# Performance work log

Hardware: AMD Instinct MI355X
Metric: run time of the kernel (lower is better)

Reference implementation:

```python
import jax, jax.numpy as jnp
import numpy as np

# kernel / loss hyperparameters (from base_params)
FIT_SIGMA = 1.0
FIT_L = 1.0
MMD_SIGMA = 1.0
MMD_L = 2.0
REG_LAMBDA = 0.01

N, D = 8192, 16


def setup_inputs() -> dict:
    key = jax.random.key(0)
    k1, k2, k3 = jax.random.split(key, 3)
    X = jax.random.normal(k1, (N, D), dtype=jnp.float32)
    Y = jax.random.normal(k2, (N, D), dtype=jnp.float32)
    Lam = jax.random.normal(k3, (N, D), dtype=jnp.float32)  # nn.init.normal_ on zeros(N,d)
    return {"X": X, "Y": Y, "Lam": Lam}


def _rbf_gram(X, sigma, l):
    # k(xi, xj) = sigma^2 * exp(-||xi - xj||^2 / (2 l^2)), vectorized over all pairs
    sq = jnp.sum(X * X, axis=1)                      # [N]
    d2 = sq[:, None] + sq[None, :] - 2.0 * (X @ X.T)  # [N, N] squared distances
    d2 = jnp.maximum(d2, 0.0)
    return (sigma ** 2) * jnp.exp(-d2 / (2.0 * l ** 2))


def reference(X, Y, Lam):
    fit_kXX = _rbf_gram(X, FIT_SIGMA, FIT_L)   # [N, N]
    mmd_kXX = _rbf_gram(X, MMD_SIGMA, MMD_L)   # [N, N]
    diff = fit_kXX @ Lam - Y                   # [N, d]
    # trace(diff^T K diff) = sum(diff * (K @ diff))
    loss_fit = jnp.sum(diff * (mmd_kXX @ diff))
    loss_reg = REG_LAMBDA * jnp.sum(Lam * (fit_kXX @ Lam))
    return loss_fit + loss_reg
```

## Files before the change

### kernel.cpp

```cpp
#include <hip/hip_runtime.h>

#define NPTS 8192
#define DIM  16

constexpr int BLK = 256;
constexpr int NIB = NPTS / BLK;

#define REG_LAMBDA 0.01f
#define C1 1.2011224087864498f
#define C2 0.6005612043932249f

typedef _Float16 h4 __attribute__((ext_vector_type(4)));
typedef float    f4 __attribute__((ext_vector_type(4)));

#define MFMA16(a, b, c) __builtin_amdgcn_mfma_f32_16x16x16f16((a), (b), (c), 0, 0, 0)

#if __has_builtin(__builtin_amdgcn_exp2f)
#define EXP2(x) __builtin_amdgcn_exp2f(x)
#else
#define EXP2(x) exp2f(x)
#endif

__device__ __forceinline__ float dot4(float4 a, float4 b) {
  return fmaf(a.x, b.x, fmaf(a.y, b.y, fmaf(a.z, b.z, a.w * b.w)));
}
__device__ __forceinline__ void add4(float4& a, float4 b) {
  a.x += b.x; a.y += b.y; a.z += b.z; a.w += b.w;
}

__device__ __forceinline__ float block_sum(float v, float* wbuf) {
#pragma unroll
  for (int o = 32; o > 0; o >>= 1) v += __shfl_down(v, o, 64);
  const int lane = threadIdx.x & 63;
  const int wid  = threadIdx.x >> 6;
  __syncthreads();
  if (lane == 0) wbuf[wid] = v;
  __syncthreads();
  float s = 0.f;
  if (threadIdx.x == 0) {
#pragma unroll
    for (int w = 0; w < BLK / 64; ++w) s += wbuf[w];
  }
  return s;
}

__global__ __launch_bounds__(BLK) void k_prep(
    const float4* __restrict__ Xv, const float4* __restrict__ Lv,
    _Float16* __restrict__ Xh1, _Float16* __restrict__ Xh2,
    _Float16* __restrict__ LamT,
    float* __restrict__ csq1, float* __restrict__ csq2,
    float* __restrict__ accums) {
  if (blockIdx.x == 0 && threadIdx.x == 0) {
    accums[0] = 0.f; accums[1] = 0.f;
  }
  const int i = blockIdx.x * BLK + threadIdx.x;
  float sq1 = 0.f, sq2 = 0.f;
  h4* x1 = (h4*)(Xh1 + (size_t)i * DIM);
  h4* x2 = (h4*)(Xh2 + (size_t)i * DIM);
#pragma unroll
  for (int q = 0; q < 4; ++q) {
    const float4 v = Xv[(size_t)i * 4 + q];
    h4 a = {(_Float16)(C1 * v.x), (_Float16)(C1 * v.y),
            (_Float16)(C1 * v.z), (_Float16)(C1 * v.w)};
    h4 b = {(_Float16)(C2 * v.x), (_Float16)(C2 * v.y),
            (_Float16)(C2 * v.z), (_Float16)(C2 * v.w)};
    x1[q] = a; x2[q] = b;
#pragma unroll
    for (int t = 0; t < 4; ++t) {
      const float fa = (float)a[t], fb = (float)b[t];
      sq1 = fmaf(fa, fa, sq1);
      sq2 = fmaf(fb, fb, sq2);
    }
    const float4 l = Lv[(size_t)i * 4 + q];
    LamT[(size_t)(4 * q + 0) * NPTS + i] = (_Float16)l.x;
    LamT[(size_t)(4 * q + 1) * NPTS + i] = (_Float16)l.y;
    LamT[(size_t)(4 * q + 2) * NPTS + i] = (_Float16)l.z;
    LamT[(size_t)(4 * q + 3) * NPTS + i] = (_Float16)l.w;
  }
  csq1[i] = -0.5f * sq1;
  csq2[i] = -0.5f * sq2;
}

__global__ __launch_bounds__(BLK) void k_pass1(
    const _Float16* __restrict__ Xh1, const _Float16* __restrict__ LamT,
    const float* __restrict__ csq1, float* __restrict__ Upart, int span) {
  const int lane = threadIdx.x & 63;
  const int w    = threadIdx.x >> 6;
  const int l16  = lane & 15;
  const int quad = lane >> 4;

  const int i0 = blockIdx.x * 256 + w * 64;
  h4 bxi[4];
  float ci[4];
#pragma unroll
  for (int t = 0; t < 4; ++t) {
    bxi[t] = *(const h4*)(Xh1 + (size_t)(i0 + 16 * t + l16) * DIM + quad * 4);
    ci[t]  = csq1[i0 + 16 * t + l16];
  }
  const _Float16* blrow = LamT + (size_t)l16 * NPTS;

  f4 U[4] = {{0.f, 0.f, 0.f, 0.f}, {0.f, 0.f, 0.f, 0.f},
             {0.f, 0.f, 0.f, 0.f}, {0.f, 0.f, 0.f, 0.f}};
  const int jbeg = blockIdx.y * span;
  const int jend = jbeg + span;
#pragma unroll 4
  for (int j0 = jbeg; j0 < jend; j0 += 16) {
    const h4 axj = *(const h4*)(Xh1 + (size_t)(j0 + l16) * DIM + quad * 4);
    const float4 cjf = *(const float4*)(csq1 + j0 + quad * 4);
    const h4 bl = *(const h4*)(blrow + j0 + quad * 4);
#pragma unroll
    for (int t = 0; t < 4; ++t) {
      const f4 cc = {cjf.x + ci[t], cjf.y + ci[t], cjf.z + ci[t], cjf.w + ci[t]};
      const f4 p = MFMA16(axj, bxi[t], cc);
      h4 ap;
#pragma unroll
      for (int r = 0; r < 4; ++r) ap[r] = (_Float16)EXP2(p[r]);
      U[t] = MFMA16(ap, bl, U[t]);
    }
  }

  float* dst = Upart + ((size_t)blockIdx.y * NPTS + i0) * DIM;
#pragma unroll
  for (int t = 0; t < 4; ++t)
#pragma unroll
    for (int r = 0; r < 4; ++r)
      dst[(16 * t + quad * 4 + r) * DIM + l16] = U[t][r];
}

__global__ __launch_bounds__(BLK) void k_reduce(
    const float4* __restrict__ Upart, const float4* __restrict__ Yv,
    const float4* __restrict__ Lv, _Float16* __restrict__ Dh,
    float* __restrict__ accums, int jc) {
  __shared__ float wred[BLK / 64];
  const int t = blockIdx.x * BLK + threadIdx.x;
  const int i = t >> 2, q = t & 3;
  float4 u = {0.f, 0.f, 0.f, 0.f};
  for (int c = 0; c < jc; ++c)
    add4(u, Upart[((size_t)c * NPTS + i) * 4 + q]);
  const float4 y = Yv[(size_t)i * 4 + q];
  h4 d = {(_Float16)(u.x - y.x), (_Float16)(u.y - y.y),
          (_Float16)(u.z - y.z), (_Float16)(u.w - y.w)};
  *(h4*)(Dh + (size_t)i * DIM + q * 4) = d;
  const float regp = dot4(Lv[(size_t)i * 4 + q], u);
  const float rtot = block_sum(regp, wred);
  if (threadIdx.x == 0) unsafeAtomicAdd(&accums[1], rtot);
}

__global__ __launch_bounds__(BLK) void k_pass2(
    const _Float16* __restrict__ Xh2, const _Float16* __restrict__ Dh,
    const float* __restrict__ csq2, float* __restrict__ accums, int span) {
  __shared__ float wred[BLK / 64];
  const int lane = threadIdx.x & 63;
  const int w    = threadIdx.x >> 6;
  const int l16  = lane & 15;
  const int quad = lane >> 4;
  const f4 fz = {0.f, 0.f, 0.f, 0.f};

  const int i0 = blockIdx.x * 256 + w * 64;
  h4 ax[4], ad[4];
  float4 cif[4];
#pragma unroll
  for (int t = 0; t < 4; ++t) {
    ax[t] = *(const h4*)(Xh2 + (size_t)(i0 + 16 * t + l16) * DIM + quad * 4);
    ad[t] = *(const h4*)(Dh  + (size_t)(i0 + 16 * t + l16) * DIM + quad * 4);
    cif[t] = *(const float4*)(csq2 + i0 + 16 * t + quad * 4);
  }

  float s = 0.f;
  const int jbeg = blockIdx.y * span;
  const int jend = jbeg + span;
#pragma unroll 4
  for (int j0 = jbeg; j0 < jend; j0 += 16) {
    const h4 bx = *(const h4*)(Xh2 + (size_t)(j0 + l16) * DIM + quad * 4);
    const h4 bd = *(const h4*)(Dh  + (size_t)(j0 + l16) * DIM + quad * 4);
    const float cj = csq2[j0 + l16];
#pragma unroll
    for (int t = 0; t < 4; ++t) {
      const f4 cc = {cif[t].x + cj, cif[t].y + cj, cif[t].z + cj, cif[t].w + cj};
      const f4 dx = MFMA16(ax[t], bx, cc);
      const f4 dd = MFMA16(ad[t], bd, fz);
#pragma unroll
      for (int r = 0; r < 4; ++r) s = fmaf(EXP2(dx[r]), dd[r], s);
    }
  }

  const float stot = block_sum(s, wred);
  if (threadIdx.x == 0) unsafeAtomicAdd(&accums[0], stot);
}

__global__ void k_final(const float* __restrict__ accums, float* __restrict__ out) {
  out[0] = accums[0] + REG_LAMBDA * accums[1];
}

extern "C" void kernel_launch(void* const* d_in, const int* in_sizes, int n_in,
                              void* d_out, int out_size, void* d_ws, size_t ws_size,
                              hipStream_t stream) {
  const float4* Xv = (const float4*)d_in[0];
  const float4* Yv = (const float4*)d_in[1];
  const float4* Lv = (const float4*)d_in[2];
  float* out = (float*)d_out;

  char* base = (char*)d_ws;
  _Float16* Xh1  = (_Float16*)(base);
  _Float16* Xh2  = (_Float16*)(base + 256 * 1024);
  _Float16* LamT = (_Float16*)(base + 512 * 1024);
  _Float16* Dh   = (_Float16*)(base + 768 * 1024);
  float*    csq1 = (float*)(base + 1024 * 1024);
  float*    csq2 = (float*)(base + 1056 * 1024);
  float*    accums = (float*)(base + 1088 * 1024);
  float*    Upart  = (float*)(base + 1088 * 1024 + 256);
  const size_t fixed = 1088 * 1024 + 256;

  int jc = 64;
  while (jc > 1 && fixed + (size_t)jc * NPTS * DIM * 4 > ws_size) jc >>= 1;
  const int span1 = NPTS / jc;
  const int jc2 = 64, span2 = NPTS / jc2;

  k_prep<<<NIB, BLK, 0, stream>>>(Xv, Lv, Xh1, Xh2, LamT, csq1, csq2, accums);
  k_pass1<<<dim3(NPTS / 256, jc), BLK, 0, stream>>>(Xh1, LamT, csq1, Upart, span1);
  k_reduce<<<NPTS * 4 / BLK, BLK, 0, stream>>>((const float4*)Upart, Yv, Lv, Dh, accums, jc);
  k_pass2<<<dim3(NPTS / 256, jc2), BLK, 0, stream>>>(Xh2, Dh, csq2, accums, span2);
  k_final<<<1, 1, 0, stream>>>(accums, out);
}
```

Baseline: 135.8 us.

## Exploit kernel symmetry in MMD pass, fuse final reduction, prefetch loop loads

The second pass now evaluates only the upper-triangular block pairs of the symmetric MMD Gram quadratic form, weighting off-diagonal pairs by two, which roughly halves its exp/MFMA work. The final scalar combine is folded into pass2 using an atomic completion counter, which removes a separate launch. Both MFMA loops prefetch the next iteration's operands into registers, and pass1 uses fewer j-chunks. The costs are some idle blocks in the pass2 grid and an extra fence and atomic per block.

```diff
diff --git a/kernel.cpp b/kernel.cpp
--- a/kernel.cpp
+++ b/kernel.cpp
@@ -50,9 +50,7 @@
     _Float16* __restrict__ LamT,
     float* __restrict__ csq1, float* __restrict__ csq2,
     float* __restrict__ accums) {
-  if (blockIdx.x == 0 && threadIdx.x == 0) {
-    accums[0] = 0.f; accums[1] = 0.f;
-  }
+  if (blockIdx.x == 0 && threadIdx.x < 4) accums[threadIdx.x] = 0.f;
   const int i = blockIdx.x * BLK + threadIdx.x;
   float sq1 = 0.f, sq2 = 0.f;
   h4* x1 = (h4*)(Xh1 + (size_t)i * DIM);
@@ -103,11 +101,19 @@
              {0.f, 0.f, 0.f, 0.f}, {0.f, 0.f, 0.f, 0.f}};
   const int jbeg = blockIdx.y * span;
   const int jend = jbeg + span;
-#pragma unroll 4
+
+  h4 axj_n = *(const h4*)(Xh1 + (size_t)(jbeg + l16) * DIM + quad * 4);
+  float4 cjf_n = *(const float4*)(csq1 + jbeg + quad * 4);
+  h4 bl_n = *(const h4*)(blrow + jbeg + quad * 4);
+
   for (int j0 = jbeg; j0 < jend; j0 += 16) {
-    const h4 axj = *(const h4*)(Xh1 + (size_t)(j0 + l16) * DIM + quad * 4);
-    const float4 cjf = *(const float4*)(csq1 + j0 + quad * 4);
-    const h4 bl = *(const h4*)(blrow + j0 + quad * 4);
+    const h4 axj = axj_n;
+    const float4 cjf = cjf_n;
+    const h4 bl = bl_n;
+    const int jn = (j0 + 16 < jend) ? j0 + 16 : jbeg;
+    axj_n = *(const h4*)(Xh1 + (size_t)(jn + l16) * DIM + quad * 4);
+    cjf_n = *(const float4*)(csq1 + jn + quad * 4);
+    bl_n  = *(const h4*)(blrow + jn + quad * 4);
 #pragma unroll
     for (int t = 0; t < 4; ++t) {
       const f4 cc = {cjf.x + ci[t], cjf.y + ci[t], cjf.z + ci[t], cjf.w + ci[t]};
@@ -148,48 +154,75 @@
 
 __global__ __launch_bounds__(BLK) void k_pass2(
     const _Float16* __restrict__ Xh2, const _Float16* __restrict__ Dh,
-    const float* __restrict__ csq2, float* __restrict__ accums, int span) {
+    const float* __restrict__ csq2, float* __restrict__ accums,
+    float* __restrict__ out) {
   __shared__ float wred[BLK / 64];
-  const int lane = threadIdx.x & 63;
-  const int w    = threadIdx.x >> 6;
-  const int l16  = lane & 15;
-  const int quad = lane >> 4;
-  const f4 fz = {0.f, 0.f, 0.f, 0.f};
-
-  const int i0 = blockIdx.x * 256 + w * 64;
-  h4 ax[4], ad[4];
-  float4 cif[4];
-#pragma unroll
-  for (int t = 0; t < 4; ++t) {
-    ax[t] = *(const h4*)(Xh2 + (size_t)(i0 + 16 * t + l16) * DIM + quad * 4);
-    ad[t] = *(const h4*)(Dh  + (size_t)(i0 + 16 * t + l16) * DIM + quad * 4);
-    cif[t] = *(const float4*)(csq2 + i0 + 16 * t + quad * 4);
-  }
-
-  float s = 0.f;
-  const int jbeg = blockIdx.y * span;
-  const int jend = jbeg + span;
-#pragma unroll 4
-  for (int j0 = jbeg; j0 < jend; j0 += 16) {
-    const h4 bx = *(const h4*)(Xh2 + (size_t)(j0 + l16) * DIM + quad * 4);
-    const h4 bd = *(const h4*)(Dh  + (size_t)(j0 + l16) * DIM + quad * 4);
-    const float cj = csq2[j0 + l16];
+  const int bi   = blockIdx.x;
+  const int k    = blockIdx.y >> 1;
+  const int half = blockIdx.y & 1;
+  const bool active = !(k == 16 && bi >= 16);
+
+  if (active) {
+    const int bj = (bi + k) & 31;
+    const float weight = (k == 0) ? 1.f : 2.f;
+    const int lane = threadIdx.x & 63;
+    const int w    = threadIdx.x >> 6;
+    const int l16  = lane & 15;
+    const int quad = lane >> 4;
+    const f4 fz = {0.f, 0.f, 0.f, 0.f};
+
+    const int i0 = bi * 256 + w * 64;
+    h4 ax[4], ad[4];
+    float4 cif[4];
 #pragma unroll
     for (int t = 0; t < 4; ++t) {
-      const f4 cc = {cif[t].x + cj, cif[t].y + cj, cif[t].z + cj, cif[t].w + cj};
-      const f4 dx = MFMA16(ax[t], bx, cc);
-      const f4 dd = MFMA16(ad[t], bd, fz);
-#pragma unroll
-      for (int r = 0; r < 4; ++r) s = fmaf(EXP2(dx[r]), dd[r], s);
-    }
-  }
-
-  const float stot = block_sum(s, wred);
-  if (threadIdx.x == 0) unsafeAtomicAdd(&accums[0], stot);
-}
-
-__global__ void k_final(const float* __restrict__ accums, float* __restrict__ out) {
-  out[0] = accums[0] + REG_LAMBDA * accums[1];
+      ax[t] = *(const h4*)(Xh2 + (size_t)(i0 + 16 * t + l16) * DIM + quad * 4);
+      ad[t] = *(const h4*)(Dh  + (size_t)(i0 + 16 * t + l16) * DIM + quad * 4);
+      cif[t] = *(const float4*)(csq2 + i0 + 16 * t + quad * 4);
+    }
+
+    float s = 0.f;
+    const int jbeg = bj * 256 + half * 128;
+    const int jend = jbeg + 128;
+
+    h4 bx_n = *(const h4*)(Xh2 + (size_t)(jbeg + l16) * DIM + quad * 4);
+    h4 bd_n = *(const h4*)(Dh  + (size_t)(jbeg + l16) * DIM + quad * 4);
+    float cj_n = csq2[jbeg + l16];
+
+    for (int j0 = jbeg; j0 < jend; j0 += 16) {
+      const h4 bx = bx_n;
+      const h4 bd = bd_n;
+      const float cj = cj_n;
+      const int jn = (j0 + 16 < jend) ? j0 + 16 : jbeg;
+      bx_n = *(const h4*)(Xh2 + (size_t)(jn + l16) * DIM + quad * 4);
+      bd_n = *(const h4*)(Dh  + (size_t)(jn + l16) * DIM + quad * 4);
+      cj_n = csq2[jn + l16];
+#pragma unroll
+      for (int t = 0; t < 4; ++t) {
+        const f4 cc = {cif[t].x + cj, cif[t].y + cj, cif[t].z + cj, cif[t].w + cj};
+        const f4 dx = MFMA16(ax[t], bx, cc);
+        const f4 dd = MFMA16(ad[t], bd, fz);
+#pragma unroll
+        for (int r = 0; r < 4; ++r) s = fmaf(EXP2(dx[r]), dd[r], s);
+      }
+    }
+
+    const float stot = block_sum(s * weight, wred);
+    if (threadIdx.x == 0) unsafeAtomicAdd(&accums[0], stot);
+  }
+
+  __threadfence();
+  if (threadIdx.x == 0) {
+    unsigned* cnt = (unsigned*)&accums[2];
+    const unsigned old = atomicAdd(cnt, 1u);
+    if (old == gridDim.x * gridDim.y - 1) {
+      const float a0 = __hip_atomic_load(&accums[0], __ATOMIC_ACQUIRE,
+                                         __HIP_MEMORY_SCOPE_AGENT);
+      const float a1 = __hip_atomic_load(&accums[1], __ATOMIC_ACQUIRE,
+                                         __HIP_MEMORY_SCOPE_AGENT);
+      out[0] = a0 + REG_LAMBDA * a1;
+    }
+  }
 }
 
 extern "C" void kernel_launch(void* const* d_in, const int* in_sizes, int n_in,
@@ -211,14 +244,12 @@
   float*    Upart  = (float*)(base + 1088 * 1024 + 256);
   const size_t fixed = 1088 * 1024 + 256;
 
-  int jc = 64;
+  int jc = 32;
   while (jc > 1 && fixed + (size_t)jc * NPTS * DIM * 4 > ws_size) jc >>= 1;
   const int span1 = NPTS / jc;
-  const int jc2 = 64, span2 = NPTS / jc2;
 
   k_prep<<<NIB, BLK, 0, stream>>>(Xv, Lv, Xh1, Xh2, LamT, csq1, csq2, accums);
   k_pass1<<<dim3(NPTS / 256, jc), BLK, 0, stream>>>(Xh1, LamT, csq1, Upart, span1);
   k_reduce<<<NPTS * 4 / BLK, BLK, 0, stream>>>((const float4*)Upart, Yv, Lv, Dh, accums, jc);
-  k_pass2<<<dim3(NPTS / 256, jc2), BLK, 0, stream>>>(Xh2, Dh, csq2, accums, span2);
-  k_final<<<1, 1, 0, stream>>>(accums, out);
-}
+  k_pass2<<<dim3(32, 34), BLK, 0, stream>>>(Xh2, Dh, csq2, accums, out);
+}
```

Result: slower. 183.9 us (+35.4%).
